# Kernel tuning notes

Measured on AMD Instinct MI355X. Metric: run time of the kernel, lower is better.

Reference implementation:

```python
import jax, jax.numpy as jnp
import numpy as np

POOL = (4000, 4000, 4000)
N_GO = 12000
N_GENES = 20000
IN_F = 8
F = 64
B = 8
D_ATT = 5
L_DIM = 16
N_LAST = 4000
EPS = 1e-5


def _seg(v, ids, n):
    # v: [B, E, ...] -> segment-sum over axis 1
    return jax.vmap(lambda a: jax.ops.segment_sum(a, ids, num_segments=n))(v)


def _ln_nodes(x, g, b):
    # torch does LayerNorm(N) on x.permute(0,2,1): normalize over the NODE axis
    mu = x.mean(axis=1, keepdims=True)
    var = x.var(axis=1, keepdims=True)
    return (x - mu) * jax.lax.rsqrt(var + EPS) * g[None, :, None] + b[None, :, None]


def _bn(x, g, b):
    # BatchNorm1d, training-mode statistics (biased var); channel axis = 1
    if x.ndim == 2:
        mu = x.mean(axis=0)
        var = x.var(axis=0)
        return (x - mu) * jax.lax.rsqrt(var + EPS) * g + b
    mu = x.mean(axis=(0, 2), keepdims=True)
    var = x.var(axis=(0, 2), keepdims=True)
    return (x - mu) * jax.lax.rsqrt(var + EPS) * g[None, :, None] + b[None, :, None]


def _enc(x, src, dst, n, w_inc, w_s, w_att_in, w_att_s, g, b):
    x_in = x @ w_inc.T                 # [B,n,F]
    x_s = x @ w_s.T
    f1 = w_inc.shape[0]
    # W_att_in([x_src; x_dst]) == x_src @ W[:, :f1].T + x_dst @ W[:, f1:].T (GAT trick)
    a_src = x_in @ w_att_in[0, :f1]    # [B,n]
    a_dst = x_in @ w_att_in[0, f1:]
    v = jnp.exp(jnp.tanh(a_src[:, src] + a_dst[:, dst]))   # [B,E]
    vn = v / _seg(v, src, n)[:, src]                        # row-normalized attention
    x_incoming = _seg(vn[:, :, None] * x_in[:, dst, :], src, n)
    v_s = jax.nn.sigmoid(x_s @ w_att_s[0])                  # [B,n]
    out = x_incoming + x_s * v_s[:, :, None]
    return jax.nn.relu(_ln_nodes(out, g, b))


def _dec(x, src, dst, n_rows, offset, w_out, w_sout, g, b):
    x_out = x @ w_out.T
    x_s = x @ w_sout.T
    deg = jax.ops.segment_sum(jnp.ones(src.shape, x.dtype), src, num_segments=n_rows)
    v = 1.0 / deg[src]                                      # [E]
    x_outgoing = _seg(v[None, :, None] * x_out[:, dst, :], src, n_rows)
    out = x_outgoing.at[:, offset:, :].add(x_s)
    return jax.nn.relu(_ln_nodes(out, g, b))


def _forward(data, t, t_D,
             w_inc0, w_inc1, w_s0, w_s1, w_att_in0, w_att_in1, w_att_s0, w_att_s1,
             gb_g0, gb_b0, gb_g1, gb_b1,
             w_out0, w_out1, w_sout0, w_sout1,
             gbd_g0, gbd_b0, gbd_g1, gbd_b1,
             catt_w, catt_bn_g, catt_bn_b,
             conc_w, b_bn_g, b_bn_b,
             concd_w, bd_bn_g, bd_bn_b,
             lat_w1, lat_bn1_g, lat_bn1_b, lat_w2, lat_bn2_g, lat_bn2_b,
             Ag_row, Ag_col,
             enc_src0, enc_dst0, enc_src1, enc_dst1,
             dec_src0, dec_dst0, dec_src1, dec_dst1):
    # initial SNP->GO sparse embedding, one sparse matrix per input channel
    gathered = data[:, Ag_col]                         # [B,nnz]
    msg0 = gathered[:, :, None] * t.T[None, :, :]      # [B,nnz,IN_F]
    x = _seg(msg0, Ag_row, N_GO)                       # [B,N_GO,IN_F]

    # encoder (attention GCN + pooling)
    x = _enc(x, enc_src0, enc_dst0, N_GO, w_inc0, w_s0, w_att_in0, w_att_s0, gb_g0, gb_b0)
    x = x[:, POOL[0]:, :]
    x = _enc(x, enc_src1, enc_dst1, N_GO - POOL[0], w_inc1, w_s1, w_att_in1, w_att_s1, gb_g1, gb_b1)
    x = x[:, POOL[1]:, :]                              # [B,N_LAST,F]

    atten_out = jax.nn.relu(_bn(x @ catt_w.T, catt_bn_g, catt_bn_b))   # [B,N_LAST,D_ATT]
    inp_out = jax.nn.relu(_bn((x @ conc_w.T)[..., 0], b_bn_g, b_bn_b)) # [B,N_LAST]

    # decoder (degree-normalized unpooling)
    x = _dec(x, dec_src0, dec_dst0, POOL[1] + POOL[2], POOL[1], w_out0, w_sout0, gbd_g0, gbd_b0)
    x = _dec(x, dec_src1, dec_dst1, N_GO, POOL[0], w_out1, w_sout1, gbd_g1, gbd_b1)

    out_D = jax.nn.relu(_bn((x @ concd_w.T)[..., 0], bd_bn_g, bd_bn_b))  # [B,N_GO]
    x_D = _seg(out_D[:, Ag_row] * t_D[None, :], Ag_col, N_GENES)          # [B,N_GENES]

    h = jax.nn.relu(_bn(inp_out @ lat_w1.T, lat_bn1_g, lat_bn1_b))
    latent = jax.nn.relu(_bn(h @ lat_w2.T, lat_bn2_g, lat_bn2_b))         # [B,L_DIM]
    return latent, x_D, atten_out


def setup_inputs():
    rng = np.random.default_rng(0)
    # GO-GO adjacency edges (row-major unique, like coalesce)
    e = np.unique(rng.integers(0, N_GO, 144000).astype(np.int64) * N_GO
                  + rng.integers(0, N_GO, 144000))
    r = (e // N_GO).astype(np.int32)
    c = (e % N_GO).astype(np.int32)
    p0, p1 = POOL[0], POOL[0] + POOL[1]
    m = (r >= p0) & (c >= p0)
    enc_src1, enc_dst1 = r[m] - p0, c[m] - p0
    ti, tj = c, r                                  # edges of A.T
    m0 = (ti >= p0) & (tj >= p1)
    dec_src0, dec_dst0 = ti[m0] - p0, tj[m0] - p1
    m1 = tj >= p0
    dec_src1, dec_dst1 = ti[m1], tj[m1] - p0
    # gene <-> GO incidence
    eg = np.unique(rng.integers(0, N_GO, 240000).astype(np.int64) * N_GENES
                   + rng.integers(0, N_GENES, 240000))
    Ag_row = (eg // N_GENES).astype(np.int32)
    Ag_col = (eg % N_GENES).astype(np.int32)
    nnz = Ag_row.shape[0]

    ks = iter(jax.random.split(jax.random.key(0), 40))

    def nrm(shape, s=0.05):
        return jax.random.normal(next(ks), shape, jnp.float32) * s

    return {
        'data': nrm((B, N_GENES), 1.0),
        't': 1.0 + nrm((IN_F, nnz), 0.1),
        't_D': 1.0 + nrm((nnz,), 0.1),
        'w_inc0': nrm((F, IN_F)), 'w_inc1': nrm((F, F)),
        'w_s0': nrm((F, IN_F)), 'w_s1': nrm((F, F)),
        'w_att_in0': nrm((1, 2 * F)), 'w_att_in1': nrm((1, 2 * F)),
        'w_att_s0': nrm((1, F)), 'w_att_s1': nrm((1, F)),
        'gb_g0': jnp.ones(N_GO), 'gb_b0': jnp.zeros(N_GO),
        'gb_g1': jnp.ones(N_GO - p0), 'gb_b1': jnp.zeros(N_GO - p0),
        'w_out0': nrm((F, F)), 'w_out1': nrm((IN_F, F)),
        'w_sout0': nrm((F, F)), 'w_sout1': nrm((IN_F, F)),
        'gbd_g0': jnp.ones(POOL[1] + POOL[2]), 'gbd_b0': jnp.zeros(POOL[1] + POOL[2]),
        'gbd_g1': jnp.ones(N_GO), 'gbd_b1': jnp.zeros(N_GO),
        'catt_w': nrm((D_ATT, F)), 'catt_bn_g': jnp.ones(N_LAST), 'catt_bn_b': jnp.zeros(N_LAST),
        'conc_w': nrm((1, F)), 'b_bn_g': jnp.ones(N_LAST), 'b_bn_b': jnp.zeros(N_LAST),
        'concd_w': nrm((1, IN_F)), 'bd_bn_g': jnp.ones(N_GO), 'bd_bn_b': jnp.zeros(N_GO),
        'lat_w1': nrm((32, N_LAST)), 'lat_bn1_g': jnp.ones(32), 'lat_bn1_b': jnp.zeros(32),
        'lat_w2': nrm((L_DIM, 32)), 'lat_bn2_g': jnp.ones(L_DIM), 'lat_bn2_b': jnp.zeros(L_DIM),
        'Ag_row': jnp.asarray(Ag_row), 'Ag_col': jnp.asarray(Ag_col),
        'enc_src0': jnp.asarray(r), 'enc_dst0': jnp.asarray(c),
        'enc_src1': jnp.asarray(enc_src1), 'enc_dst1': jnp.asarray(enc_dst1),
        'dec_src0': jnp.asarray(dec_src0), 'dec_dst0': jnp.asarray(dec_dst0),
        'dec_src1': jnp.asarray(dec_src1), 'dec_dst1': jnp.asarray(dec_dst1),
    }


def reference(data, t, t_D,
              w_inc0, w_inc1, w_s0, w_s1, w_att_in0, w_att_in1, w_att_s0, w_att_s1,
              gb_g0, gb_b0, gb_g1, gb_b1,
              w_out0, w_out1, w_sout0, w_sout1,
              gbd_g0, gbd_b0, gbd_g1, gbd_b1,
              catt_w, catt_bn_g, catt_bn_b,
              conc_w, b_bn_g, b_bn_b,
              concd_w, bd_bn_g, bd_bn_b,
              lat_w1, lat_bn1_g, lat_bn1_b, lat_w2, lat_bn2_g, lat_bn2_b,
              Ag_row, Ag_col,
              enc_src0, enc_dst0, enc_src1, enc_dst1,
              dec_src0, dec_dst0, dec_src1, dec_dst1):
    return _forward(data, t, t_D,
                    w_inc0, w_inc1, w_s0, w_s1, w_att_in0, w_att_in1, w_att_s0, w_att_s1,
                    gb_g0, gb_b0, gb_g1, gb_b1,
                    w_out0, w_out1, w_sout0, w_sout1,
                    gbd_g0, gbd_b0, gbd_g1, gbd_b1,
                    catt_w, catt_bn_g, catt_bn_b,
                    conc_w, b_bn_g, b_bn_b,
                    concd_w, bd_bn_g, bd_bn_b,
                    lat_w1, lat_bn1_g, lat_bn1_b, lat_w2, lat_bn2_g, lat_bn2_b,
                    Ag_row, Ag_col,
                    enc_src0, enc_dst0, enc_src1, enc_dst1,
                    dec_src0, dec_dst0, dec_src1, dec_dst1)
```

## Files before the change

### kernel.cpp

```cpp
#include <hip/hip_runtime.h>
#include <math.h>

#define BB 8
#define N_GO 12000
#define N_GENES 20000
#define IN_F 8
#define FF 64
#define D_ATT 5
#define L_DIM 16
#define N_LAST 4000
#define P0_ 4000
#define EPSF 1e-5f

__global__ void k_row_bounds(const int* __restrict__ src, int* __restrict__ rs,
                             int* __restrict__ re, int E) {
    int e = blockIdx.x * 256 + threadIdx.x;
    if (e >= E) return;
    int r = src[e];
    if (e == 0 || src[e - 1] != r) rs[r] = e;
    if (e == E - 1 || src[e + 1] != r) re[r] = e + 1;
}

__global__ void k_gene2go_w(const float* __restrict__ data, const float* __restrict__ t,
                            const int* __restrict__ col, const int* __restrict__ rs,
                            const int* __restrict__ re, float* __restrict__ x0, int nnz) {
    int wid = blockIdx.x * 4 + (threadIdx.x >> 6);
    if (wid >= N_GO) return;
    int lane = threadIdx.x & 63;
    int f = lane & 7, eo = lane >> 3;
    int e0 = rs[wid], e1 = re[wid];
    float acc[BB];
#pragma unroll
    for (int b = 0; b < BB; b++) acc[b] = 0.f;
    for (int e = e0; e < e1; e += 8) {
        int ee = e + eo;
        bool ok = ee < e1;
        int ec = ok ? ee : (e1 - 1);
        int c = col[ec];
        float tv = ok ? t[(size_t)f * nnz + ee] : 0.f;
#pragma unroll
        for (int b = 0; b < BB; b++)
            acc[b] += tv * data[b * N_GENES + c];
    }
#pragma unroll
    for (int b = 0; b < BB; b++) {
        acc[b] += __shfl_xor(acc[b], 8);
        acc[b] += __shfl_xor(acc[b], 16);
        acc[b] += __shfl_xor(acc[b], 32);
    }
    if (lane < IN_F) {
#pragma unroll
        for (int b = 0; b < BB; b++)
            x0[((size_t)b * N_GO + wid) * IN_F + lane] = acc[b];
    }
}

template<int FIN, bool SCAL>
__global__ __launch_bounds__(256, 2)
void k_linear2_att(const float* __restrict__ X, const float* __restrict__ W1,
                   const float* __restrict__ W2, const float* __restrict__ watt,
                   const float* __restrict__ ws, float* __restrict__ Y1,
                   float* __restrict__ Y2, float* __restrict__ ASRC,
                   float* __restrict__ ADST, float* __restrict__ VS,
                   int n_nodes, long xbs, int xoff, int total_waves) {
    __shared__ float w1s[FIN * FF];
    __shared__ float w2s[FIN * FF];
    int lane = threadIdx.x & 63;
    for (int i = threadIdx.x; i < FIN * FF; i += 256) {
        int fo = i / FIN, k = i % FIN;
        w1s[k * FF + fo] = W1[i];
        w2s[k * FF + fo] = W2[i];
    }
    __syncthreads();
    float w1r[FIN], w2r[FIN];
#pragma unroll
    for (int k = 0; k < FIN; k++) {
        w1r[k] = w1s[k * FF + lane];
        w2r[k] = w2s[k * FF + lane];
    }
    float wa = 0.f, wb = 0.f, wc = 0.f;
    if (SCAL) { wa = watt[lane]; wb = watt[FF + lane]; wc = ws[lane]; }
    int wid = blockIdx.x * 4 + (threadIdx.x >> 6);
    for (int n = wid; n < n_nodes; n += total_waves) {
        for (int b = 0; b < BB; b++) {
            const float* xr = X + (size_t)b * xbs + (size_t)(n + xoff) * FIN;
            float a1 = 0.f, a2 = 0.f;
#pragma unroll
            for (int k = 0; k < FIN; k += 4) {
                float4 x = *(const float4*)(xr + k);
                a1 += x.x * w1r[k] + x.y * w1r[k + 1] + x.z * w1r[k + 2] + x.w * w1r[k + 3];
                a2 += x.x * w2r[k] + x.y * w2r[k + 1] + x.z * w2r[k + 2] + x.w * w2r[k + 3];
            }
            Y1[((size_t)b * n_nodes + n) * FF + lane] = a1;
            Y2[((size_t)b * n_nodes + n) * FF + lane] = a2;
            if (SCAL) {
                float s0 = a1 * wa, s1 = a1 * wb, s2 = a2 * wc;
                for (int m = 1; m < 64; m <<= 1) {
                    s0 += __shfl_xor(s0, m);
                    s1 += __shfl_xor(s1, m);
                    s2 += __shfl_xor(s2, m);
                }
                if (lane == 0) {
                    ASRC[b * n_nodes + n] = s0;
                    ADST[b * n_nodes + n] = s1;
                    VS[b * n_nodes + n] = 1.f / (1.f + expf(-s2));
                }
            }
        }
    }
}

__global__ __launch_bounds__(256, 2)
void k_linear2_reg8(const float* __restrict__ X, const float* __restrict__ W1,
                    const float* __restrict__ W2, float* __restrict__ Y1,
                    float* __restrict__ Y2, int n_nodes, long xbs, int xoff,
                    int total_waves) {
    __shared__ float w1s[FF * IN_F];
    __shared__ float w2s[FF * IN_F];
    int lane = threadIdx.x & 63;
    for (int i = threadIdx.x; i < FF * IN_F; i += 256) {
        int fo = i / FF, k = i % FF;
        w1s[k * IN_F + fo] = W1[i];
        w2s[k * IN_F + fo] = W2[i];
    }
    __syncthreads();
    int of = lane & 7;
    int slot = lane >> 3;
    float w1r[FF], w2r[FF];
#pragma unroll
    for (int k = 0; k < FF; k++) {
        w1r[k] = w1s[k * IN_F + of];
        w2r[k] = w2s[k * IN_F + of];
    }
    int wid = blockIdx.x * 4 + (threadIdx.x >> 6);
    for (long n0 = (long)wid * 8; n0 < n_nodes; n0 += (long)total_waves * 8) {
        int n = (int)n0 + slot;
        bool ok = (n < n_nodes);
        int nn = ok ? n : (n_nodes - 1);
        for (int b = 0; b < BB; b++) {
            const float* xr = X + (size_t)b * xbs + (size_t)(nn + xoff) * FF;
            float a1 = 0.f, a2 = 0.f;
#pragma unroll
            for (int k = 0; k < FF; k += 4) {
                float4 x = *(const float4*)(xr + k);
                a1 += x.x * w1r[k] + x.y * w1r[k + 1] + x.z * w1r[k + 2] + x.w * w1r[k + 3];
                a2 += x.x * w2r[k] + x.y * w2r[k + 1] + x.z * w2r[k + 2] + x.w * w2r[k + 3];
            }
            if (ok) {
                Y1[((size_t)b * n_nodes + n) * IN_F + of] = a1;
                Y2[((size_t)b * n_nodes + n) * IN_F + of] = a2;
            }
        }
    }
}

__global__ void k_edge_v(const float* __restrict__ a_src, const float* __restrict__ a_dst,
                         const int* __restrict__ src, const int* __restrict__ dst,
                         float* __restrict__ v, int E, int n_nodes) {
    int e = blockIdx.x * 256 + threadIdx.x;
    if (e >= E) return;
    int b = blockIdx.y;
    v[(size_t)b * E + e] = expf(tanhf(a_src[b * n_nodes + src[e]] + a_dst[b * n_nodes + dst[e]]));
}

__global__ void k_agg_enc_f(const float* __restrict__ Xin, const float* __restrict__ Xs,
                            const float* __restrict__ EDGEV, const float* __restrict__ VS,
                            const int* __restrict__ dst, const int* __restrict__ rs,
                            const int* __restrict__ re, float* __restrict__ Out,
                            float* __restrict__ sums, int n_nodes, int E, int nblk) {
    int b = blockIdx.x & 7;
    int wid = threadIdx.x >> 6;
    int lane = threadIdx.x & 63;
    const float* Xb  = Xin + (size_t)b * n_nodes * FF;
    const float* Xsb = Xs  + (size_t)b * n_nodes * FF;
    const float* vv  = EDGEV + (size_t)b * E;
    float s1 = 0.f, s2 = 0.f;
    for (int r = (blockIdx.x >> 3) * 4 + wid; r < n_nodes; r += nblk * 4) {
        int e0 = rs[r], e1 = re[r];
        float sv0 = 0.f, sv1 = 0.f, acc0 = 0.f, acc1 = 0.f;
        int e = e0;
        for (; e + 1 < e1; e += 2) {
            int d0 = dst[e], d1 = dst[e + 1];
            float v0 = vv[e], v1 = vv[e + 1];
            sv0 += v0; sv1 += v1;
            acc0 += v0 * Xb[(size_t)d0 * FF + lane];
            acc1 += v1 * Xb[(size_t)d1 * FF + lane];
        }
        if (e < e1) {
            int d0 = dst[e];
            float v0 = vv[e];
            sv0 += v0;
            acc0 += v0 * Xb[(size_t)d0 * FF + lane];
        }
        float sv = sv0 + sv1, acc = acc0 + acc1;
        float o = (e1 > e0) ? acc / sv : 0.f;
        o += Xsb[(size_t)r * FF + lane] * VS[b * n_nodes + r];
        Out[((size_t)b * n_nodes + r) * FF + lane] = o;
        s1 += o; s2 += o * o;
    }
    __shared__ float sh1[4][64], sh2[4][64];
    sh1[wid][lane] = s1; sh2[wid][lane] = s2;
    __syncthreads();
    if (wid == 0) {
        float a = sh1[0][lane] + sh1[1][lane] + sh1[2][lane] + sh1[3][lane];
        float c = sh2[0][lane] + sh2[1][lane] + sh2[2][lane] + sh2[3][lane];
        atomicAdd(&sums[(b * FF + lane) * 2],     a);
        atomicAdd(&sums[(b * FF + lane) * 2 + 1], c);
    }
}

__global__ void k_ln_stats(const float* __restrict__ X, float* __restrict__ sums,
                           int n_nodes, int Fdim, int npb) {
    int b = blockIdx.y;
    int f = threadIdx.x & (Fdim - 1);
    int nl = threadIdx.x / Fdim;
    int stride = 256 / Fdim;
    int n0 = blockIdx.x * npb;
    int n1 = n0 + npb; if (n1 > n_nodes) n1 = n_nodes;
    const float* xb = X + (size_t)b * n_nodes * Fdim;
    float s1 = 0.f, s2 = 0.f;
    for (int n = n0 + nl; n < n1; n += stride) {
        float x = xb[(size_t)n * Fdim + f];
        s1 += x; s2 += x * x;
    }
    __shared__ float sh1[256], sh2[256];
    sh1[threadIdx.x] = s1; sh2[threadIdx.x] = s2;
    __syncthreads();
    for (int o = 128; o >= Fdim; o >>= 1) {
        if (threadIdx.x < o) { sh1[threadIdx.x] += sh1[threadIdx.x + o]; sh2[threadIdx.x] += sh2[threadIdx.x + o]; }
        __syncthreads();
    }
    if (threadIdx.x < Fdim) {
        atomicAdd(&sums[(b * Fdim + threadIdx.x) * 2],     sh1[threadIdx.x]);
        atomicAdd(&sums[(b * Fdim + threadIdx.x) * 2 + 1], sh2[threadIdx.x]);
    }
}

__global__ void k_ln_apply_relu(const float* __restrict__ X, const float* __restrict__ sums,
                                const float* __restrict__ g, const float* __restrict__ bb,
                                float* __restrict__ Y, int n_nodes, int Fdim) {
    long idx = (long)blockIdx.x * 256 + threadIdx.x;
    if (idx >= (long)n_nodes * Fdim) return;
    int b = blockIdx.y;
    int n = (int)(idx / Fdim);
    int f = (int)(idx % Fdim);
    float s1 = sums[(b * Fdim + f) * 2], s2 = sums[(b * Fdim + f) * 2 + 1];
    float mu = s1 / n_nodes;
    float var = s2 / n_nodes - mu * mu;
    float rs = rsqrtf(var + EPSF);
    size_t o = (size_t)b * n_nodes * Fdim + idx;
    float y = (X[o] - mu) * rs * g[n] + bb[n];
    Y[o] = fmaxf(y, 0.f);
}

__global__ void k_deg_i(const int* __restrict__ src, int* __restrict__ deg, int E) {
    int e = blockIdx.x * 256 + threadIdx.x;
    if (e < E) atomicAdd(&deg[src[e]], 1);
}

__global__ void k_scan(const int* __restrict__ deg, int* __restrict__ rsd,
                       int* __restrict__ cursor, int n) {
    __shared__ int part[1024];
    int t = threadIdx.x;
    int chunk = (n + 1023) >> 10;
    int s0 = t * chunk, s1 = s0 + chunk; if (s1 > n) s1 = n;
    int s = 0;
    for (int i = s0; i < s1 && i < n; i++) s += deg[i];
    part[t] = s;
    __syncthreads();
    for (int o = 1; o < 1024; o <<= 1) {
        int v = (t >= o) ? part[t - o] : 0;
        __syncthreads();
        part[t] += v;
        __syncthreads();
    }
    int base = (t == 0) ? 0 : part[t - 1];
    for (int i = s0; i < s1 && i < n; i++) {
        rsd[i] = base; cursor[i] = base;
        base += deg[i];
    }
    if (t == 1023) rsd[n] = part[1023];
}

__global__ void k_scatter(const int* __restrict__ src, const int* __restrict__ dst,
                          int* __restrict__ cursor, int* __restrict__ csrd, int E) {
    int e = blockIdx.x * 256 + threadIdx.x;
    if (e >= E) return;
    int pos = atomicAdd(&cursor[src[e]], 1);
    csrd[pos] = dst[e];
}

__global__ void k_agg_dec64(const float* __restrict__ Xout, const float* __restrict__ Xs,
                            const int* __restrict__ rsd, const int* __restrict__ csrd,
                            float* __restrict__ Out, float* __restrict__ sums,
                            int n_rows, int n_in, int offset, int nblk) {
    int b = blockIdx.x & 7;
    int wid = threadIdx.x >> 6;
    int lane = threadIdx.x & 63;
    const float* Xb = Xout + (size_t)b * n_in * FF;
    int nxs = n_rows - offset;
    const float* Xsb = Xs + (size_t)b * nxs * FF;
    float s1 = 0.f, s2 = 0.f;
    for (int r = (blockIdx.x >> 3) * 4 + wid; r < n_rows; r += nblk * 4) {
        int e0 = rsd[r], e1 = rsd[r + 1];
        float acc0 = 0.f, acc1 = 0.f;
        int e = e0;
        for (; e + 1 < e1; e += 2) {
            acc0 += Xb[(size_t)csrd[e] * FF + lane];
            acc1 += Xb[(size_t)csrd[e + 1] * FF + lane];
        }
        if (e < e1) acc0 += Xb[(size_t)csrd[e] * FF + lane];
        float acc = acc0 + acc1;
        float o = (e1 > e0) ? acc / (float)(e1 - e0) : 0.f;
        if (r >= offset)
            o += Xsb[(size_t)(r - offset) * FF + lane];
        Out[((size_t)b * n_rows + r) * FF + lane] = o;
        s1 += o; s2 += o * o;
    }
    __shared__ float sh1[4][64], sh2[4][64];
    sh1[wid][lane] = s1; sh2[wid][lane] = s2;
    __syncthreads();
    if (wid == 0) {
        float a = sh1[0][lane] + sh1[1][lane] + sh1[2][lane] + sh1[3][lane];
        float c = sh2[0][lane] + sh2[1][lane] + sh2[2][lane] + sh2[3][lane];
        atomicAdd(&sums[(b * FF + lane) * 2],     a);
        atomicAdd(&sums[(b * FF + lane) * 2 + 1], c);
    }
}

__global__ void k_agg_dec8(const float* __restrict__ Xout, const float* __restrict__ Xs,
                           const int* __restrict__ rsd, const int* __restrict__ csrd,
                           float* __restrict__ Out, int n_rows, int n_in, int offset) {
    int r = blockIdx.x * 4 + (threadIdx.x >> 6);
    if (r >= n_rows) return;
    int lane = threadIdx.x & 63;
    int f = lane & 7, slot = lane >> 3;
    int e0 = rsd[r], e1 = rsd[r + 1];
    float acc[BB];
#pragma unroll
    for (int b = 0; b < BB; b++) acc[b] = 0.f;
    for (int e = e0 + slot; e < e1; e += 8) {
        int d = csrd[e];
#pragma unroll
        for (int b = 0; b < BB; b++)
            acc[b] += Xout[((size_t)b * n_in + d) * IN_F + f];
    }
#pragma unroll
    for (int b = 0; b < BB; b++) {
        acc[b] += __shfl_xor(acc[b], 8);
        acc[b] += __shfl_xor(acc[b], 16);
        acc[b] += __shfl_xor(acc[b], 32);
    }
    float coef = (e1 > e0) ? 1.f / (float)(e1 - e0) : 0.f;
    int nxs = n_rows - offset;
    if (lane < IN_F) {
#pragma unroll
        for (int b = 0; b < BB; b++) {
            float o = acc[b] * coef;
            if (r >= offset)
                o += Xs[((size_t)b * nxs + (r - offset)) * IN_F + lane];
            Out[((size_t)b * n_rows + r) * IN_F + lane] = o;
        }
    }
}

__global__ void k_heads(const float* __restrict__ X, const float* __restrict__ Wa,
                        const float* __restrict__ wc, const float* __restrict__ ga,
                        const float* __restrict__ ba, const float* __restrict__ gc,
                        const float* __restrict__ bc, float* __restrict__ ATT,
                        float* __restrict__ INP, long xbs, int xoff) {
    int i = blockIdx.x * 4 + (threadIdx.x >> 6);
    if (i >= N_LAST) return;
    int lane = threadIdx.x & 63;
    float w0 = Wa[0 * FF + lane], w1 = Wa[1 * FF + lane], w2 = Wa[2 * FF + lane];
    float w3 = Wa[3 * FF + lane], w4 = Wa[4 * FF + lane];
    float wcv = wc[lane];
    float y[BB][D_ATT], yc[BB];
    float s1 = 0.f, s2 = 0.f;
#pragma unroll
    for (int b = 0; b < BB; b++) {
        float x = X[(size_t)b * xbs + (size_t)(i + xoff) * FF + lane];
        float p0 = x * w0, p1 = x * w1, p2 = x * w2, p3 = x * w3, p4 = x * w4, pc = x * wcv;
        for (int m = 1; m < 64; m <<= 1) {
            p0 += __shfl_xor(p0, m); p1 += __shfl_xor(p1, m); p2 += __shfl_xor(p2, m);
            p3 += __shfl_xor(p3, m); p4 += __shfl_xor(p4, m); pc += __shfl_xor(pc, m);
        }
        y[b][0] = p0; y[b][1] = p1; y[b][2] = p2; y[b][3] = p3; y[b][4] = p4;
        yc[b] = pc;
        s1 += p0 + p1 + p2 + p3 + p4;
        s2 += p0 * p0 + p1 * p1 + p2 * p2 + p3 * p3 + p4 * p4;
    }
    const float cnt = (float)(BB * D_ATT);
    float mu = s1 / cnt, var = s2 / cnt - mu * mu;
    float rsv = rsqrtf(var + EPSF);
    float gg = ga[i], bv = ba[i];
#pragma unroll
    for (int b = 0; b < BB; b++) {
        float yv = lane == 0 ? y[b][0] : lane == 1 ? y[b][1] : lane == 2 ? y[b][2]
                 : lane == 3 ? y[b][3] : y[b][4];
        if (lane < D_ATT)
            ATT[((size_t)b * N_LAST + i) * D_ATT + lane] = fmaxf((yv - mu) * rsv * gg + bv, 0.f);
    }
    float c1 = 0.f, c2 = 0.f;
#pragma unroll
    for (int b = 0; b < BB; b++) { c1 += yc[b]; c2 += yc[b] * yc[b]; }
    float muc = c1 / BB, varc = c2 / BB - muc * muc;
    float rc = rsqrtf(varc + EPSF);
    float ggc = gc[i], bvc = bc[i];
    if (lane < BB) {
        float v = lane == 0 ? yc[0] : lane == 1 ? yc[1] : lane == 2 ? yc[2] : lane == 3 ? yc[3]
                : lane == 4 ? yc[4] : lane == 5 ? yc[5] : lane == 6 ? yc[6] : yc[7];
        INP[(size_t)lane * N_LAST + i] = fmaxf((v - muc) * rc * ggc + bvc, 0.f);
    }
}

template<int FIN>
__global__ void k_head_scalar(const float* __restrict__ X, const float* __restrict__ w,
                              const float* __restrict__ g, const float* __restrict__ bb,
                              float* __restrict__ Z, int n_nodes, long xbs, int xoff) {
    int i = blockIdx.x * 256 + threadIdx.x;
    if (i >= n_nodes) return;
    float y[BB];
    float s1 = 0.f, s2 = 0.f;
    const float4* wr = (const float4*)w;
    for (int b = 0; b < BB; b++) {
        const float4* xr = (const float4*)(X + (size_t)b * xbs + (size_t)(i + xoff) * FIN);
        float acc = 0.f;
#pragma unroll
        for (int q = 0; q < FIN / 4; q++) {
            float4 x = xr[q], u = wr[q];
            acc += x.x * u.x + x.y * u.y + x.z * u.z + x.w * u.w;
        }
        y[b] = acc; s1 += acc; s2 += acc * acc;
    }
    float mu = s1 / BB, var = s2 / BB - mu * mu;
    float rs = rsqrtf(var + EPSF);
    float gg = g[i], bv = bb[i];
    for (int b = 0; b < BB; b++)
        Z[(size_t)b * n_nodes + i] = fmaxf((y[b] - mu) * rs * gg + bv, 0.f);
}

__global__ void k_xd(const float* __restrict__ outD, const float* __restrict__ tD,
                     const int* __restrict__ row, const int* __restrict__ col,
                     float* __restrict__ xD, int nnz) {
    int e = blockIdx.x * 256 + threadIdx.x;
    if (e >= nnz) return;
    int b = blockIdx.y;
    atomicAdd(&xD[(size_t)b * N_GENES + col[e]], outD[(size_t)b * N_GO + row[e]] * tD[e]);
}

__global__ void k_lat1(const float* __restrict__ INP, const float* __restrict__ W,
                       const float* __restrict__ g, const float* __restrict__ bb,
                       float* __restrict__ H1R) {
    int j = blockIdx.x;
    int w = threadIdx.x >> 6;
    int lane = threadIdx.x & 63;
    const float* xr = INP + (size_t)w * N_LAST;
    const float* wr = W + (size_t)j * N_LAST;
    float s = 0.f;
    for (int k = lane; k < N_LAST; k += 64) s += xr[k] * wr[k];
    for (int o = 32; o > 0; o >>= 1) s += __shfl_down(s, o);
    __shared__ float sh[BB];
    if (lane == 0) sh[w] = s;
    __syncthreads();
    if (threadIdx.x < BB) {
        float s1 = 0.f, s2 = 0.f;
        for (int q = 0; q < BB; q++) { float y = sh[q]; s1 += y; s2 += y * y; }
        float mu = s1 / BB, var = s2 / BB - mu * mu;
        float rs = rsqrtf(var + EPSF);
        H1R[threadIdx.x * 32 + j] = fmaxf((sh[threadIdx.x] - mu) * rs * g[j] + bb[j], 0.f);
    }
}

__global__ void k_lat2(const float* __restrict__ H1R, const float* __restrict__ W2,
                       const float* __restrict__ g, const float* __restrict__ bb,
                       float* __restrict__ out_lat) {
    int b = threadIdx.x >> 4, j = threadIdx.x & 15;
    float acc = 0.f;
    for (int k = 0; k < 32; k++) acc += H1R[b * 32 + k] * W2[j * 32 + k];
    __shared__ float sh[128];
    sh[threadIdx.x] = acc;
    __syncthreads();
    float s1 = 0.f, s2 = 0.f;
    for (int q = 0; q < BB; q++) { float y = sh[q * 16 + j]; s1 += y; s2 += y * y; }
    float mu = s1 / BB, var = s2 / BB - mu * mu;
    float rs = rsqrtf(var + EPSF);
    out_lat[b * 16 + j] = fmaxf((acc - mu) * rs * g[j] + bb[j], 0.f);
}

extern "C" void kernel_launch(void* const* d_in, const int* in_sizes, int n_in,
                              void* d_out, int out_size, void* d_ws, size_t ws_size,
                              hipStream_t stream) {
    const float* data      = (const float*)d_in[0];
    const float* t         = (const float*)d_in[1];
    const float* t_D       = (const float*)d_in[2];
    const float* w_inc0    = (const float*)d_in[3];
    const float* w_inc1    = (const float*)d_in[4];
    const float* w_s0      = (const float*)d_in[5];
    const float* w_s1      = (const float*)d_in[6];
    const float* w_att_in0 = (const float*)d_in[7];
    const float* w_att_in1 = (const float*)d_in[8];
    const float* w_att_s0  = (const float*)d_in[9];
    const float* w_att_s1  = (const float*)d_in[10];
    const float* gb_g0     = (const float*)d_in[11];
    const float* gb_b0     = (const float*)d_in[12];
    const float* gb_g1     = (const float*)d_in[13];
    const float* gb_b1     = (const float*)d_in[14];
    const float* w_out0    = (const float*)d_in[15];
    const float* w_out1    = (const float*)d_in[16];
    const float* w_sout0   = (const float*)d_in[17];
    const float* w_sout1   = (const float*)d_in[18];
    const float* gbd_g0    = (const float*)d_in[19];
    const float* gbd_b0    = (const float*)d_in[20];
    const float* gbd_g1    = (const float*)d_in[21];
    const float* gbd_b1    = (const float*)d_in[22];
    const float* catt_w    = (const float*)d_in[23];
    const float* catt_bn_g = (const float*)d_in[24];
    const float* catt_bn_b = (const float*)d_in[25];
    const float* conc_w    = (const float*)d_in[26];
    const float* b_bn_g    = (const float*)d_in[27];
    const float* b_bn_b    = (const float*)d_in[28];
    const float* concd_w   = (const float*)d_in[29];
    const float* bd_bn_g   = (const float*)d_in[30];
    const float* bd_bn_b   = (const float*)d_in[31];
    const float* lat_w1    = (const float*)d_in[32];
    const float* lat_bn1_g = (const float*)d_in[33];
    const float* lat_bn1_b = (const float*)d_in[34];
    const float* lat_w2    = (const float*)d_in[35];
    const float* lat_bn2_g = (const float*)d_in[36];
    const float* lat_bn2_b = (const float*)d_in[37];
    const int* Ag_row   = (const int*)d_in[38];
    const int* Ag_col   = (const int*)d_in[39];
    const int* enc_src0 = (const int*)d_in[40];
    const int* enc_dst0 = (const int*)d_in[41];
    const int* enc_src1 = (const int*)d_in[42];
    const int* enc_dst1 = (const int*)d_in[43];
    const int* dec_src0 = (const int*)d_in[44];
    const int* dec_dst0 = (const int*)d_in[45];
    const int* dec_src1 = (const int*)d_in[46];
    const int* dec_dst1 = (const int*)d_in[47];

    const int nnz = in_sizes[2];
    const int E0  = in_sizes[40];
    const int E1  = in_sizes[42];
    const int ED0 = in_sizes[44];
    const int ED1 = in_sizes[46];
    const int EDMAX = (ED0 > ED1 ? ED0 : ED1);

    char* wsb = (char*)d_ws;
    size_t off = 0;
    auto alloc = [&](size_t bytes) -> void* {
        void* p = wsb + off;
        off += (bytes + 255) & ~(size_t)255;
        return p;
    };
    const size_t ARENA = (size_t)BB * N_GO * FF;
    float* P0 = (float*)alloc(ARENA * 4);
    float* P1 = (float*)alloc(ARENA * 4);
    float* P2 = (float*)alloc(ARENA * 4);
    float* P3 = (float*)alloc(ARENA * 4);
    float* EDGEV = (float*)alloc((size_t)BB * E0 * 4);
    float* ASRC = (float*)alloc((size_t)BB * N_GO * 4);
    float* ADST = (float*)alloc((size_t)BB * N_GO * 4);
    float* VS   = (float*)alloc((size_t)BB * N_GO * 4);
    float* SUMS = (float*)alloc(2 * BB * FF * 4);
    float* INP  = (float*)alloc((size_t)BB * N_LAST * 4);
    float* OUTD = (float*)alloc((size_t)BB * N_GO * 4);
    float* H1R  = (float*)alloc(BB * 32 * 4);
    int* RS   = (int*)alloc(N_GO * 4);
    int* RE   = (int*)alloc(N_GO * 4);
    int* DEGI = (int*)alloc(N_GO * 4);
    int* RSD  = (int*)alloc((N_GO + 1) * 4);
    int* CURS = (int*)alloc(N_GO * 4);
    int* CSRD = (int*)alloc((size_t)EDMAX * 4);

    float* out_lat = (float*)d_out;
    float* out_xd  = out_lat + BB * L_DIM;
    float* out_att = out_xd + (size_t)BB * N_GENES;

    dim3 blk(256);
    auto g1 = [](long n) { return dim3((unsigned)((n + 255) / 256)); };
    auto g2 = [](long n, int y) { return dim3((unsigned)((n + 255) / 256), (unsigned)y); };
    auto gw = [](int n) { return dim3((unsigned)((n + 3) / 4)); };
    const int LNB = 1024;
    const int LWAVES = LNB * 4;
    const int ANB = 256;
    const int N1 = N_GO - P0_;

    hipMemsetAsync(RS, 0, N_GO * 4, stream);
    hipMemsetAsync(RE, 0, N_GO * 4, stream);
    k_row_bounds<<<g1(nnz), blk, 0, stream>>>(Ag_row, RS, RE, nnz);
    k_gene2go_w<<<gw(N_GO), blk, 0, stream>>>(data, t, Ag_col, RS, RE, P0, nnz);

    k_linear2_att<IN_F, true><<<dim3(LNB), blk, 0, stream>>>(P0, w_inc0, w_s0, w_att_in0, w_att_s0,
        P1, P2, ASRC, ADST, VS, N_GO, (long)N_GO * IN_F, 0, LWAVES);
    hipMemsetAsync(RS, 0, N_GO * 4, stream);
    hipMemsetAsync(RE, 0, N_GO * 4, stream);
    k_row_bounds<<<g1(E0), blk, 0, stream>>>(enc_src0, RS, RE, E0);
    k_edge_v<<<g2(E0, BB), blk, 0, stream>>>(ASRC, ADST, enc_src0, enc_dst0, EDGEV, E0, N_GO);
    hipMemsetAsync(SUMS, 0, 2 * BB * FF * 4, stream);
    k_agg_enc_f<<<dim3(ANB * 8), blk, 0, stream>>>(P1, P2, EDGEV, VS, enc_dst0, RS, RE, P3, SUMS, N_GO, E0, ANB);
    k_ln_apply_relu<<<g2((long)N_GO * FF, BB), blk, 0, stream>>>(P3, SUMS, gb_g0, gb_b0, P0, N_GO, FF);

    k_linear2_att<FF, true><<<dim3(LNB), blk, 0, stream>>>(P0, w_inc1, w_s1, w_att_in1, w_att_s1,
        P1, P2, ASRC, ADST, VS, N1, (long)N_GO * FF, P0_, LWAVES);
    hipMemsetAsync(RS, 0, N_GO * 4, stream);
    hipMemsetAsync(RE, 0, N_GO * 4, stream);
    k_row_bounds<<<g1(E1), blk, 0, stream>>>(enc_src1, RS, RE, E1);
    k_edge_v<<<g2(E1, BB), blk, 0, stream>>>(ASRC, ADST, enc_src1, enc_dst1, EDGEV, E1, N1);
    hipMemsetAsync(SUMS, 0, 2 * BB * FF * 4, stream);
    k_agg_enc_f<<<dim3(ANB * 8), blk, 0, stream>>>(P1, P2, EDGEV, VS, enc_dst1, RS, RE, P3, SUMS, N1, E1, ANB);
    k_ln_apply_relu<<<g2((long)N1 * FF, BB), blk, 0, stream>>>(P3, SUMS, gb_g1, gb_b1, P0, N1, FF);

    k_heads<<<gw(N_LAST), blk, 0, stream>>>(P0, catt_w, conc_w, catt_bn_g, catt_bn_b,
                                            b_bn_g, b_bn_b, out_att, INP, (long)N1 * FF, P0_);

    k_linear2_att<FF, false><<<dim3(LNB), blk, 0, stream>>>(P0, w_out0, w_sout0, nullptr, nullptr,
        P1, P2, nullptr, nullptr, nullptr, N_LAST, (long)N1 * FF, P0_, LWAVES);
    hipMemsetAsync(DEGI, 0, 8000 * 4, stream);
    k_deg_i<<<g1(ED0), blk, 0, stream>>>(dec_src0, DEGI, ED0);
    k_scan<<<dim3(1), dim3(1024), 0, stream>>>(DEGI, RSD, CURS, 8000);
    k_scatter<<<g1(ED0), blk, 0, stream>>>(dec_src0, dec_dst0, CURS, CSRD, ED0);
    hipMemsetAsync(SUMS, 0, 2 * BB * FF * 4, stream);
    k_agg_dec64<<<dim3(ANB * 8), blk, 0, stream>>>(P1, P2, RSD, CSRD, P3, SUMS, 8000, N_LAST, 4000, ANB);
    k_ln_apply_relu<<<g2((long)8000 * FF, BB), blk, 0, stream>>>(P3, SUMS, gbd_g0, gbd_b0, P0, 8000, FF);

    k_linear2_reg8<<<dim3(LNB), blk, 0, stream>>>(P0, w_out1, w_sout1, P1, P2, 8000, (long)8000 * FF, 0, LWAVES);
    hipMemsetAsync(DEGI, 0, N_GO * 4, stream);
    k_deg_i<<<g1(ED1), blk, 0, stream>>>(dec_src1, DEGI, ED1);
    k_scan<<<dim3(1), dim3(1024), 0, stream>>>(DEGI, RSD, CURS, N_GO);
    k_scatter<<<g1(ED1), blk, 0, stream>>>(dec_src1, dec_dst1, CURS, CSRD, ED1);
    k_agg_dec8<<<gw(N_GO), blk, 0, stream>>>(P1, P2, RSD, CSRD, P3, N_GO, 8000, 4000);
    hipMemsetAsync(SUMS, 0, 2 * BB * IN_F * 4, stream);
    k_ln_stats<<<dim3((N_GO + 511) / 512, BB), blk, 0, stream>>>(P3, SUMS, N_GO, IN_F, 512);
    k_ln_apply_relu<<<g2((long)N_GO * IN_F, BB), blk, 0, stream>>>(P3, SUMS, gbd_g1, gbd_b1, P0, N_GO, IN_F);

    k_head_scalar<IN_F><<<g1(N_GO), blk, 0, stream>>>(P0, concd_w, bd_bn_g, bd_bn_b, OUTD, N_GO, (long)N_GO * IN_F, 0);
    hipMemsetAsync(out_xd, 0, (size_t)BB * N_GENES * 4, stream);
    k_xd<<<g2(nnz, BB), blk, 0, stream>>>(OUTD, t_D, Ag_row, Ag_col, out_xd, nnz);

    k_lat1<<<dim3(32), dim3(512), 0, stream>>>(INP, lat_w1, lat_bn1_g, lat_bn1_b, H1R);
    k_lat2<<<dim3(1), dim3(128), 0, stream>>>(H1R, lat_w2, lat_bn2_g, lat_bn2_b, out_lat);

    (void)n_in; (void)out_size; (void)ws_size;
}
```

Baseline: 568.4 us.

## Replace atomic gene scatter with column-CSR gather for decoder output

The final gene-space projection no longer scatters atomically over all nonzeros for every batch. It now builds a column-keyed CSR on the device (degree count, scan, scatter of row index and t_D value), then gathers with one wavefront per gene covering all 8 batches and reduces with shuffles. This removes float atomics and the output memset. In exchange it adds three kernels that build the CSR on every call, including a single-block scan over 20000 genes, and the scatter order within a column is nondeterministic.

```diff
diff --git a/kernel.cpp b/kernel.cpp
--- a/kernel.cpp
+++ b/kernel.cpp
@@ -290,6 +290,34 @@
     csrd[pos] = dst[e];
 }
 
+__global__ void k_scatter2(const int* __restrict__ key, const int* __restrict__ row,
+                           const float* __restrict__ tD, int* __restrict__ cursor,
+                           int* __restrict__ csrr, float* __restrict__ csrt, int E) {
+    int e = blockIdx.x * 256 + threadIdx.x;
+    if (e >= E) return;
+    int pos = atomicAdd(&cursor[key[e]], 1);
+    csrr[pos] = row[e];
+    csrt[pos] = tD[e];
+}
+
+__global__ void k_xd_g(const float* __restrict__ outD, const int* __restrict__ rsg,
+                       const int* __restrict__ csrr, const float* __restrict__ csrt,
+                       float* __restrict__ xD) {
+    int g = blockIdx.x * 4 + (threadIdx.x >> 6);
+    if (g >= N_GENES) return;
+    int lane = threadIdx.x & 63;
+    int b = lane & 7, slot = lane >> 3;
+    int e0 = rsg[g], e1 = rsg[g + 1];
+    float acc = 0.f;
+    for (int e = e0 + slot; e < e1; e += 8)
+        acc += csrt[e] * outD[(size_t)b * N_GO + csrr[e]];
+    acc += __shfl_xor(acc, 8);
+    acc += __shfl_xor(acc, 16);
+    acc += __shfl_xor(acc, 32);
+    if (lane < BB)
+        xD[(size_t)b * N_GENES + g] = acc;
+}
+
 __global__ void k_agg_dec64(const float* __restrict__ Xout, const float* __restrict__ Xs,
                             const int* __restrict__ rsd, const int* __restrict__ csrd,
                             float* __restrict__ Out, float* __restrict__ sums,
@@ -438,15 +466,6 @@
     float gg = g[i], bv = bb[i];
     for (int b = 0; b < BB; b++)
         Z[(size_t)b * n_nodes + i] = fmaxf((y[b] - mu) * rs * gg + bv, 0.f);
-}
-
-__global__ void k_xd(const float* __restrict__ outD, const float* __restrict__ tD,
-                     const int* __restrict__ row, const int* __restrict__ col,
-                     float* __restrict__ xD, int nnz) {
-    int e = blockIdx.x * 256 + threadIdx.x;
-    if (e >= nnz) return;
-    int b = blockIdx.y;
-    atomicAdd(&xD[(size_t)b * N_GENES + col[e]], outD[(size_t)b * N_GO + row[e]] * tD[e]);
 }
 
 __global__ void k_lat1(const float* __restrict__ INP, const float* __restrict__ W,
@@ -545,7 +564,8 @@
     const int E1  = in_sizes[42];
     const int ED0 = in_sizes[44];
     const int ED1 = in_sizes[46];
-    const int EDMAX = (ED0 > ED1 ? ED0 : ED1);
+    int EDMAX = (ED0 > ED1 ? ED0 : ED1);
+    if (nnz > EDMAX) EDMAX = nnz;
 
     char* wsb = (char*)d_ws;
     size_t off = 0;
@@ -569,10 +589,11 @@
     float* H1R  = (float*)alloc(BB * 32 * 4);
     int* RS   = (int*)alloc(N_GO * 4);
     int* RE   = (int*)alloc(N_GO * 4);
-    int* DEGI = (int*)alloc(N_GO * 4);
-    int* RSD  = (int*)alloc((N_GO + 1) * 4);
-    int* CURS = (int*)alloc(N_GO * 4);
+    int* DEGI = (int*)alloc(N_GENES * 4);
+    int* RSD  = (int*)alloc((N_GENES + 1) * 4);
+    int* CURS = (int*)alloc(N_GENES * 4);
     int* CSRD = (int*)alloc((size_t)EDMAX * 4);
+    float* CSRT = (float*)alloc((size_t)nnz * 4);
 
     float* out_lat = (float*)d_out;
     float* out_xd  = out_lat + BB * L_DIM;
@@ -636,8 +657,11 @@
     k_ln_apply_relu<<<g2((long)N_GO * IN_F, BB), blk, 0, stream>>>(P3, SUMS, gbd_g1, gbd_b1, P0, N_GO, IN_F);
 
     k_head_scalar<IN_F><<<g1(N_GO), blk, 0, stream>>>(P0, concd_w, bd_bn_g, bd_bn_b, OUTD, N_GO, (long)N_GO * IN_F, 0);
-    hipMemsetAsync(out_xd, 0, (size_t)BB * N_GENES * 4, stream);
-    k_xd<<<g2(nnz, BB), blk, 0, stream>>>(OUTD, t_D, Ag_row, Ag_col, out_xd, nnz);
+    hipMemsetAsync(DEGI, 0, N_GENES * 4, stream);
+    k_deg_i<<<g1(nnz), blk, 0, stream>>>(Ag_col, DEGI, nnz);
+    k_scan<<<dim3(1), dim3(1024), 0, stream>>>(DEGI, RSD, CURS, N_GENES);
+    k_scatter2<<<g1(nnz), blk, 0, stream>>>(Ag_col, Ag_row, t_D, CURS, CSRD, CSRT, nnz);
+    k_xd_g<<<gw(N_GENES), blk, 0, stream>>>(OUTD, RSD, CSRD, CSRT, out_xd);
 
     k_lat1<<<dim3(32), dim3(512), 0, stream>>>(INP, lat_w1, lat_bn1_g, lat_bn1_b, H1R);
     k_lat2<<<dim3(1), dim3(128), 0, stream>>>(H1R, lat_w2, lat_bn2_g, lat_bn2_b, out_lat);
```

New measurement: 544.2 us. -4.3%, faster.
